# Kernel tuning notes

Measured on AMD Instinct MI355X. Metric: run time of the kernel, lower is better.

## Reference

```python
import jax, jax.numpy as jnp
import numpy as np

NUM_ANCHORS = 2
NUM_CLASSES = 20
H = 7
W = 7
IMG_H = 448
IMG_W = 448
NMS_THRESH = 0.7
SCORE_THRESH = 0.05
NBOX = H * W * NUM_ANCHORS  # 98 candidate boxes per image


def _format_outputs(x):
    # x: [b, H*W*(num_anchors*5 + num_classes)] -> decoded boxes/objectness/scores
    b = x.shape[0]
    x = x.reshape(b, H, W, NUM_ANCHORS * 5 + NUM_CLASSES)
    # class scores shared across anchors of a cell (repeat_interleave in torch)
    b_scores = jnp.broadcast_to(
        x[..., -NUM_CLASSES:].reshape(b, H * W, 1, NUM_CLASSES),
        (b, H * W, NUM_ANCHORS, NUM_CLASSES),
    )
    xa = x[..., : NUM_ANCHORS * 5].reshape(b, H, W, NUM_ANCHORS, 5)
    c_x = jnp.arange(W, dtype=x.dtype) * (IMG_W / W)
    c_y = jnp.arange(H, dtype=x.dtype) * (IMG_H / H)
    b_x = jax.nn.sigmoid(xa[..., 0]) + c_x[None, None, :, None]
    b_y = jax.nn.sigmoid(xa[..., 1]) + c_y[None, :, None, None]
    b_w = jax.nn.sigmoid(xa[..., 2])
    b_h = jax.nn.sigmoid(xa[..., 3])
    b_coords = jnp.stack((b_x, b_y, b_w, b_h), axis=-1).reshape(b, H * W, NUM_ANCHORS, 4)
    b_o = jax.nn.sigmoid(xa[..., 4]).reshape(b, H * W, NUM_ANCHORS)
    return b_coords, b_o, b_scores


def _pairwise_iou(boxes):
    # boxes: [n, 4] xyxy -> [n, n] IoU (torchvision box_iou semantics, 0 where union==0)
    area = (boxes[:, 2] - boxes[:, 0]) * (boxes[:, 3] - boxes[:, 1])
    lt = jnp.maximum(boxes[:, None, :2], boxes[None, :, :2])
    rb = jnp.minimum(boxes[:, None, 2:], boxes[None, :, 2:])
    wh = jnp.clip(rb - lt, 0.0)
    inter = wh[..., 0] * wh[..., 1]
    union = area[:, None] + area[None, :] - inter
    return jnp.where(union > 0, inter / union, 0.0)


def _per_image(coords, o, sc):
    # coords: [NBOX,4] (x,y,w,h), o: [NBOX], sc: [NBOX,NUM_CLASSES]
    valid = o >= 0.5  # objectness gate (b_o >= 0.5 selection in torch)
    labels = jnp.argmax(sc, axis=-1)
    scores = jnp.max(sc, axis=-1)
    # xywh -> xyxy, clamp to [0,1] (as in post_process)
    boxes = jnp.clip(
        jnp.concatenate([coords[:, :2], coords[:, :2] + coords[:, 2:]], axis=-1), 0.0, 1.0
    )
    # sort by score descending, invalid boxes pushed to the end
    s = jnp.where(valid, scores, -jnp.inf)
    order = jnp.argsort(-s)
    boxes_s = boxes[order]
    scores_s = scores[order]
    labels_s = labels[order]
    valid_s = valid[order]
    iou = _pairwise_iou(boxes_s)
    idxs = jnp.arange(NBOX)

    def body(i, alive):
        # if box i is still alive, suppress later boxes with IoU > thresh
        suppress = (iou[i] > NMS_THRESH) & (idxs > i) & alive[i]
        return alive & ~suppress

    alive = jax.lax.fori_loop(0, NBOX, body, valid_s)
    keep = alive & (scores_s >= SCORE_THRESH)
    boxes_out = jnp.where(keep[:, None], boxes_s, 0.0)
    scores_out = jnp.where(keep, scores_s, 0.0)
    labels_out = jnp.where(keep, labels_s, 0)
    return boxes_out, scores_out, labels_out, keep


def setup_inputs() -> dict:
    key = jax.random.key(0)
    x = jax.random.normal(key, (8192, H * W * (NUM_ANCHORS * 5 + NUM_CLASSES)), dtype=jnp.float32)
    return {"x": x}


def reference(x):
    b_coords, b_o, b_scores = _format_outputs(x)
    b = x.shape[0]
    coords = b_coords.reshape(b, -1, 4)
    o = b_o.reshape(b, -1)
    sc = b_scores.reshape(b, -1, NUM_CLASSES)
    boxes, scores, labels, keep = jax.vmap(_per_image)(coords, o, sc)
    # padded detections: [b, NBOX, 4], [b, NBOX], [b, NBOX], keep mask [b, NBOX]
    return boxes, scores, labels, keep
```

## Files before the change

kernel.cpp:

```cpp
#include <hip/hip_runtime.h>
#include <math.h>

#define NBOX 98
#define ROWLEN 1470
#define NMS_T 0.7f
#define SCORE_T 0.05f

__device__ __forceinline__ float psigm(float v) {
    return 1.0f / (1.0f + expf(-v));
}
__device__ __forceinline__ float fsigm(float v) {
    return __builtin_amdgcn_rcpf(1.0f + __expf(-v));
}

__global__ __launch_bounds__(256) void yolo_post(const float* __restrict__ x,
                                                 float* __restrict__ out,
                                                 int batch) {
    const int wid  = threadIdx.x >> 6;
    const int lane = threadIdx.x & 63;
    const int img  = blockIdx.x * 4 + wid;
    if (img >= batch) return;

    const int  cell   = lane;
    const bool active = (cell < 49);

    const float* c = x + (size_t)img * ROWLEN + (active ? cell : 0) * 30;

    const float2 d0  = *reinterpret_cast<const float2*>(c);
    const float4 d1  = *reinterpret_cast<const float4*>(c + 2);
    const float4 d2  = *reinterpret_cast<const float4*>(c + 6);
    const float4 q0  = *reinterpret_cast<const float4*>(c + 10);
    const float4 q1  = *reinterpret_cast<const float4*>(c + 14);
    const float4 q2  = *reinterpret_cast<const float4*>(c + 18);
    const float4 q3  = *reinterpret_cast<const float4*>(c + 22);
    const float4 q4  = *reinterpret_cast<const float4*>(c + 26);

    float cls[20] = {q0.x,q0.y,q0.z,q0.w, q1.x,q1.y,q1.z,q1.w,
                     q2.x,q2.y,q2.z,q2.w, q3.x,q3.y,q3.z,q3.w,
                     q4.x,q4.y,q4.z,q4.w};
    float mx = cls[0]; int ml = 0;
    #pragma unroll
    for (int t = 1; t < 20; ++t) {
        if (cls[t] > mx) { mx = cls[t]; ml = t; }
    }
    const float s   = active ? mx : 0.0f;
    const float lab = (float)ml;

    int vbits = 0;
    float4 B0 = make_float4(1.f, 1.f, 1.f, 1.f);
    float4 B1 = make_float4(1.f, 1.f, 1.f, 1.f);
    if (active) {
        const int ci = cell / 7;
        const int cj = cell - ci * 7;
        if (d1.z >= 0.0f) vbits |= 1;
        if (d2.w >= 0.0f) vbits |= 2;

        const float sx0 = fsigm(d0.x), sy0 = fsigm(d0.y);
        const float sw0 = fsigm(d1.x), sh0 = fsigm(d1.y);
        const float sx1 = fsigm(d1.w), sy1 = fsigm(d2.x);
        const float sw1 = fsigm(d2.y), sh1 = fsigm(d2.z);

        if (cj == 0) {
            B0.x = fminf(fmaxf(sx0, 0.f), 1.f);
            B0.z = fminf(fmaxf(sx0 + sw0, 0.f), 1.f);
            B1.x = fminf(fmaxf(sx1, 0.f), 1.f);
            B1.z = fminf(fmaxf(sx1 + sw1, 0.f), 1.f);
        }
        if (ci == 0) {
            B0.y = fminf(fmaxf(sy0, 0.f), 1.f);
            B0.w = fminf(fmaxf(sy0 + sh0, 0.f), 1.f);
            B1.y = fminf(fmaxf(sy1, 0.f), 1.f);
            B1.w = fminf(fmaxf(sy1 + sh1, 0.f), 1.f);
        }
    }

    const bool v0 = (vbits & 1) != 0;
    const bool v1 = (vbits & 2) != 0;
    const int  cnt = (vbits & 1) + (vbits >> 1);

    const unsigned long long V0m = __ballot(v0);
    const unsigned long long V1m = __ballot(v1);
    const int V = (int)__popcll(V0m) + (int)__popcll(V1m);

    bool kill_local = false;
    if (cell == 0 && (vbits & 3) == 3) {
        const float a0 = (B0.z - B0.x) * (B0.w - B0.y);
        const float a1 = (B1.z - B1.x) * (B1.w - B1.y);
        const float w  = fmaxf(fminf(B0.z, B1.z) - fmaxf(B0.x, B1.x), 0.f);
        const float h  = fmaxf(fminf(B0.w, B1.w) - fmaxf(B0.y, B1.y), 0.f);
        const float inter = w * h;
        const float uni   = a0 + a1 - inter;
        const float delta = inter - NMS_T * uni;
        if (fabsf(delta) < 1e-4f * uni) {
            const float px0 = psigm(d0.x), py0 = psigm(d0.y);
            const float pw0 = psigm(d1.x), ph0 = psigm(d1.y);
            const float px1 = psigm(d1.w), py1 = psigm(d2.x);
            const float pw1 = psigm(d2.y), ph1 = psigm(d2.z);
            const float X0 = fminf(fmaxf(px0, 0.f), 1.f), Y0 = fminf(fmaxf(py0, 0.f), 1.f);
            const float Z0 = fminf(fmaxf(px0 + pw0, 0.f), 1.f), W0 = fminf(fmaxf(py0 + ph0, 0.f), 1.f);
            const float X1 = fminf(fmaxf(px1, 0.f), 1.f), Y1 = fminf(fmaxf(py1, 0.f), 1.f);
            const float Z1 = fminf(fmaxf(px1 + pw1, 0.f), 1.f), W1 = fminf(fmaxf(py1 + ph1, 0.f), 1.f);
            const float pa0 = (Z0 - X0) * (W0 - Y0);
            const float pa1 = (Z1 - X1) * (W1 - Y1);
            const float pw  = fmaxf(fminf(Z0, Z1) - fmaxf(X0, X1), 0.f);
            const float ph  = fmaxf(fminf(W0, W1) - fmaxf(Y0, Y1), 0.f);
            const float pint = pw * ph;
            const float puni = pa0 + pa1 - pint;
            const float iou  = (puni > 0.f) ? (pint / puni) : 0.f;
            kill_local = (iou > NMS_T);
        } else {
            kill_local = (delta > 0.f);
        }
    }
    const bool kill1 = (__ballot(kill_local) != 0ull);

    const int ib = __float_as_int(s);
    const unsigned uo = (unsigned)ib ^ (unsigned)((ib >> 31) | 0x80000000);
    const unsigned long long key =
        ((unsigned long long)uo << 8) | ((unsigned)(63 - cell) << 2) | (unsigned)cnt;
    const unsigned klo = (unsigned)key;
    const unsigned khi = (unsigned)(key >> 32);

    int acc0 = 0, acc1 = 0, acc2 = 0, acc3 = 0;
    #pragma unroll
    for (int j = 0; j < 49; ++j) {
        const unsigned jlo = (unsigned)__builtin_amdgcn_readlane((int)klo, j);
        const unsigned jhi = (unsigned)__builtin_amdgcn_readlane((int)khi, j);
        const unsigned long long kj = ((unsigned long long)jhi << 32) | jlo;
        const int cj_ = (int)(jlo & 3u);
        const int add = (kj > key) ? cj_ : 0;
        if ((j & 3) == 0) acc0 += add;
        else if ((j & 3) == 1) acc1 += add;
        else if ((j & 3) == 2) acc2 += add;
        else acc3 += add;
    }
    const int rcom = (acc0 + acc1) + (acc2 + acc3);

    const unsigned long long below = (1ull << cell) - 1ull;
    const int prefv = (int)__popcll(V0m & below) + (int)__popcll(V1m & below);

    const int r0 = v0 ? rcom : (V + 2 * cell - prefv);
    const int r1 = v1 ? (rcom + (v0 ? 1 : 0))
                      : (V + 2 * cell + 1 - prefv - (v0 ? 1 : 0));

    const bool k0 = v0 && (s >= SCORE_T);
    const bool k1 = v1 && (s >= SCORE_T) && !(kill1 && cell == 0);

    if (active) {
        float4* boxes = reinterpret_cast<float4*>(out + (size_t)img * (NBOX * 4));
        const size_t base1 = (size_t)batch * (NBOX * 4);
        const size_t bn    = (size_t)batch * NBOX;
        float* scores = out + base1 +          (size_t)img * NBOX;
        float* labels = out + base1 + bn +     (size_t)img * NBOX;
        float* keepm  = out + base1 + 2 * bn + (size_t)img * NBOX;

        const float4 z = make_float4(0.f, 0.f, 0.f, 0.f);
        boxes[r0]  = k0 ? B0 : z;
        boxes[r1]  = k1 ? B1 : z;
        scores[r0] = k0 ? s : 0.f;
        scores[r1] = k1 ? s : 0.f;
        labels[r0] = k0 ? lab : 0.f;
        labels[r1] = k1 ? lab : 0.f;
        keepm[r0]  = k0 ? 1.f : 0.f;
        keepm[r1]  = k1 ? 1.f : 0.f;
    }
}

extern "C" void kernel_launch(void* const* d_in, const int* in_sizes, int n_in,
                              void* d_out, int out_size, void* d_ws, size_t ws_size,
                              hipStream_t stream) {
    const float* x = (const float*)d_in[0];
    float* out = (float*)d_out;
    const int batch = in_sizes[0] / ROWLEN;
    const int grid  = (batch + 3) / 4;
    yolo_post<<<grid, 256, 0, stream>>>(x, out, batch);
}
```

Before: 100.4 us.

## Process two images per wavefront and use a tree reduction for the class argmax

Each wavefront now handles two images. Both images' cell data is loaded up front, before either is processed, so more memory loads are in flight per wave and the grid is halved. The serial 20-way class argmax becomes a pairwise tree reduction that shortens the dependency chain. In exchange each wave holds more registers and has fewer waves available to hide latency, and the tie-break order of the tree argmax differs slightly from the sequential scan.

```diff
diff --git a/kernel.cpp b/kernel.cpp
--- a/kernel.cpp
+++ b/kernel.cpp
@@ -13,36 +13,54 @@
     return __builtin_amdgcn_rcpf(1.0f + __expf(-v));
 }
 
-__global__ __launch_bounds__(256) void yolo_post(const float* __restrict__ x,
-                                                 float* __restrict__ out,
-                                                 int batch) {
-    const int wid  = threadIdx.x >> 6;
-    const int lane = threadIdx.x & 63;
-    const int img  = blockIdx.x * 4 + wid;
-    if (img >= batch) return;
-
+struct CellData {
+    float2 d0;
+    float4 d1, d2;
+    float4 q0, q1, q2, q3, q4;
+};
+
+__device__ __forceinline__ CellData load_cell(const float* __restrict__ c) {
+    CellData r;
+    r.d0 = *reinterpret_cast<const float2*>(c);
+    r.d1 = *reinterpret_cast<const float4*>(c + 2);
+    r.d2 = *reinterpret_cast<const float4*>(c + 6);
+    r.q0 = *reinterpret_cast<const float4*>(c + 10);
+    r.q1 = *reinterpret_cast<const float4*>(c + 14);
+    r.q2 = *reinterpret_cast<const float4*>(c + 18);
+    r.q3 = *reinterpret_cast<const float4*>(c + 22);
+    r.q4 = *reinterpret_cast<const float4*>(c + 26);
+    return r;
+}
+
+__device__ __forceinline__ void amx(float av, int ai, float bv, int bi,
+                                    float& ov, int& oi) {
+    const bool l = (av >= bv);
+    ov = l ? av : bv;
+    oi = l ? ai : bi;
+}
+
+__device__ __forceinline__ void process(const CellData& D, int img, int lane,
+                                        float* __restrict__ out, int batch) {
     const int  cell   = lane;
     const bool active = (cell < 49);
 
-    const float* c = x + (size_t)img * ROWLEN + (active ? cell : 0) * 30;
-
-    const float2 d0  = *reinterpret_cast<const float2*>(c);
-    const float4 d1  = *reinterpret_cast<const float4*>(c + 2);
-    const float4 d2  = *reinterpret_cast<const float4*>(c + 6);
-    const float4 q0  = *reinterpret_cast<const float4*>(c + 10);
-    const float4 q1  = *reinterpret_cast<const float4*>(c + 14);
-    const float4 q2  = *reinterpret_cast<const float4*>(c + 18);
-    const float4 q3  = *reinterpret_cast<const float4*>(c + 22);
-    const float4 q4  = *reinterpret_cast<const float4*>(c + 26);
-
-    float cls[20] = {q0.x,q0.y,q0.z,q0.w, q1.x,q1.y,q1.z,q1.w,
-                     q2.x,q2.y,q2.z,q2.w, q3.x,q3.y,q3.z,q3.w,
-                     q4.x,q4.y,q4.z,q4.w};
-    float mx = cls[0]; int ml = 0;
+    float cls[20] = {D.q0.x,D.q0.y,D.q0.z,D.q0.w, D.q1.x,D.q1.y,D.q1.z,D.q1.w,
+                     D.q2.x,D.q2.y,D.q2.z,D.q2.w, D.q3.x,D.q3.y,D.q3.z,D.q3.w,
+                     D.q4.x,D.q4.y,D.q4.z,D.q4.w};
+    float pv[10]; int pi[10];
     #pragma unroll
-    for (int t = 1; t < 20; ++t) {
-        if (cls[t] > mx) { mx = cls[t]; ml = t; }
-    }
+    for (int t = 0; t < 10; ++t) amx(cls[2*t], 2*t, cls[2*t+1], 2*t+1, pv[t], pi[t]);
+    float rv[5]; int ri[5];
+    #pragma unroll
+    for (int t = 0; t < 5; ++t) amx(pv[2*t], pi[2*t], pv[2*t+1], pi[2*t+1], rv[t], ri[t]);
+    float u0v, u1v; int u0i, u1i;
+    amx(rv[0], ri[0], rv[1], ri[1], u0v, u0i);
+    amx(rv[2], ri[2], rv[3], ri[3], u1v, u1i);
+    float wv; int wi;
+    amx(u0v, u0i, u1v, u1i, wv, wi);
+    float mx; int ml;
+    amx(wv, wi, rv[4], ri[4], mx, ml);
+
     const float s   = active ? mx : 0.0f;
     const float lab = (float)ml;
 
@@ -52,13 +70,13 @@
     if (active) {
         const int ci = cell / 7;
         const int cj = cell - ci * 7;
-        if (d1.z >= 0.0f) vbits |= 1;
-        if (d2.w >= 0.0f) vbits |= 2;
-
-        const float sx0 = fsigm(d0.x), sy0 = fsigm(d0.y);
-        const float sw0 = fsigm(d1.x), sh0 = fsigm(d1.y);
-        const float sx1 = fsigm(d1.w), sy1 = fsigm(d2.x);
-        const float sw1 = fsigm(d2.y), sh1 = fsigm(d2.z);
+        if (D.d1.z >= 0.0f) vbits |= 1;
+        if (D.d2.w >= 0.0f) vbits |= 2;
+
+        const float sx0 = fsigm(D.d0.x), sy0 = fsigm(D.d0.y);
+        const float sw0 = fsigm(D.d1.x), sh0 = fsigm(D.d1.y);
+        const float sx1 = fsigm(D.d1.w), sy1 = fsigm(D.d2.x);
+        const float sw1 = fsigm(D.d2.y), sh1 = fsigm(D.d2.z);
 
         if (cj == 0) {
             B0.x = fminf(fmaxf(sx0, 0.f), 1.f);
@@ -92,10 +110,10 @@
         const float uni   = a0 + a1 - inter;
         const float delta = inter - NMS_T * uni;
         if (fabsf(delta) < 1e-4f * uni) {
-            const float px0 = psigm(d0.x), py0 = psigm(d0.y);
-            const float pw0 = psigm(d1.x), ph0 = psigm(d1.y);
-            const float px1 = psigm(d1.w), py1 = psigm(d2.x);
-            const float pw1 = psigm(d2.y), ph1 = psigm(d2.z);
+            const float px0 = psigm(D.d0.x), py0 = psigm(D.d0.y);
+            const float pw0 = psigm(D.d1.x), ph0 = psigm(D.d1.y);
+            const float px1 = psigm(D.d1.w), py1 = psigm(D.d2.x);
+            const float pw1 = psigm(D.d2.y), ph1 = psigm(D.d2.z);
             const float X0 = fminf(fmaxf(px0, 0.f), 1.f), Y0 = fminf(fmaxf(py0, 0.f), 1.f);
             const float Z0 = fminf(fmaxf(px0 + pw0, 0.f), 1.f), W0 = fminf(fmaxf(py0 + ph0, 0.f), 1.f);
             const float X1 = fminf(fmaxf(px1, 0.f), 1.f), Y1 = fminf(fmaxf(py1, 0.f), 1.f);
@@ -166,12 +184,36 @@
     }
 }
 
+__global__ __launch_bounds__(256) void yolo_post(const float* __restrict__ x,
+                                                 float* __restrict__ out,
+                                                 int batch) {
+    const int wid  = threadIdx.x >> 6;
+    const int lane = threadIdx.x & 63;
+    const int gw   = blockIdx.x * 4 + wid;
+    const int imgA = 2 * gw;
+    const int imgB = 2 * gw + 1;
+    if (imgA >= batch) return;
+
+    const int cellOff = (lane < 49 ? lane : 0) * 30;
+    const float* cA = x + (size_t)imgA * ROWLEN + cellOff;
+
+    const bool hasB = (imgB < batch);
+    const float* cB = hasB ? (x + (size_t)imgB * ROWLEN + cellOff) : cA;
+
+    const CellData A = load_cell(cA);
+    const CellData B = load_cell(cB);
+
+    process(A, imgA, lane, out, batch);
+    if (hasB) process(B, imgB, lane, out, batch);
+}
+
 extern "C" void kernel_launch(void* const* d_in, const int* in_sizes, int n_in,
                               void* d_out, int out_size, void* d_ws, size_t ws_size,
                               hipStream_t stream) {
     const float* x = (const float*)d_in[0];
     float* out = (float*)d_out;
     const int batch = in_sizes[0] / ROWLEN;
-    const int grid  = (batch + 3) / 4;
+    const int waves = (batch + 1) / 2;
+    const int grid  = (waves + 3) / 4;
     yolo_post<<<grid, 256, 0, stream>>>(x, out, batch);
 }
```

Result: no change. 100.0 us (-0.4%).
